# Optimization experiments

Hardware: AMD Instinct MI355X
Metric: run time of the kernel (lower is better)

The kernel has to match this reference:

```python
import jax, jax.numpy as jnp
import numpy as np

B, N, D, E = 16, 64, 512, 512
MSG = 512          # message_size must equal edge_feature_size (scatter into edge states)
LINK_H = 512       # GraphConv hidden channels
P = 2              # propagate_layers
HOI, ROLES = 26, 2


def setup_inputs() -> dict:
    key = jax.random.key(0)
    ks = jax.random.split(key, 12)
    s = 0.02
    return dict(
        edge_features=jax.random.normal(ks[0], (B, N, N, E), jnp.float32),
        node_features=jax.random.normal(ks[1], (B, N, D), jnp.float32),
        node_labels=jnp.zeros((B, N, HOI), jnp.float32),
        node_roles=jnp.zeros((B, N, ROLES), jnp.float32),
        # message_fun 'linear_concat_relu': Linear(D+E -> MSG) + ReLU
        Wm=(jax.random.normal(ks[2], (MSG, D + E), jnp.float32) * s),
        bm=jnp.zeros((MSG,), jnp.float32),
        # link_fun GraphConv: 1x1 Conv2d stack E->LINK_H->LINK_H->1
        Wl1=(jax.random.normal(ks[3], (LINK_H, E), jnp.float32) * s),
        bl1=jnp.zeros((LINK_H,), jnp.float32),
        Wl2=(jax.random.normal(ks[4], (LINK_H, LINK_H), jnp.float32) * s),
        bl2=jnp.zeros((LINK_H,), jnp.float32),
        Wlo=(jax.random.normal(ks[5], (1, LINK_H), jnp.float32) * s),
        blo=jnp.zeros((1,), jnp.float32),
        # update_fun GRU(input=MSG, hidden=D), torch gate order r,z,n
        W_ih=(jax.random.normal(ks[6], (3 * D, MSG), jnp.float32) * s),
        b_ih=jnp.zeros((3 * D,), jnp.float32),
        W_hh=(jax.random.normal(ks[7], (3 * D, D), jnp.float32) * s),
        b_hh=jnp.zeros((3 * D,), jnp.float32),
        # readout FCs
        Wr1=(jax.random.normal(ks[8], (HOI, D), jnp.float32) * s),
        br1=jnp.zeros((HOI,), jnp.float32),
        Wr2=(jax.random.normal(ks[9], (ROLES, D), jnp.float32) * s),
        br2=jnp.zeros((ROLES,), jnp.float32),
    )


def _link(x, Wl1, bl1, Wl2, bl2, Wlo, blo):
    # x: [B, C, N, N]; 1x1 conv stack -> [B, N, N]
    h = jax.nn.relu(jnp.einsum('bcvw,hc->bhvw', x, Wl1) + bl1[None, :, None, None])
    h = jax.nn.relu(jnp.einsum('bcvw,hc->bhvw', h, Wl2) + bl2[None, :, None, None])
    return (jnp.einsum('bcvw,hc->bhvw', h, Wlo) + blo[None, :, None, None])[:, 0]


def _forward(edge_features, node_features, Wm, bm, Wl1, bl1, Wl2, bl2, Wlo, blo,
             W_ih, b_ih, W_hh, b_hh, Wr1, br1, Wr2, br2):
    e = jnp.transpose(edge_features, (0, 3, 1, 2))   # [B,E,v,w]
    nf = jnp.transpose(node_features, (0, 2, 1))     # [B,D,N]
    # hidden node states are never written back in the source, so raw messages
    # m(h_w, e_vw) are constant across propagation rounds: compute once, vectorized over v.
    h_part = jnp.broadcast_to(nf[:, :, None, :], (B, D, N, N))   # h_w broadcast over v
    cat = jnp.concatenate([h_part, e], axis=1)                   # [B, D+E, v, w]
    M = jax.nn.relu(jnp.einsum('bcvw,mc->bmvw', cat, Wm) + bm[None, :, None, None])
    edge_state = e
    gated = M
    for _ in range(P):
        pred_adj = _link(edge_state, Wl1, bl1, Wl2, bl2, Wlo, blo)      # [B,v,w]
        gated = jax.nn.sigmoid(pred_adj)[:, None, :, :] * M            # [B,m,v,w]
        # source stores m_v into hidden_edge_states[..., :, :, i_node] (column v)
        edge_state = jnp.swapaxes(gated, 2, 3)
    m_sum = jnp.sum(gated, axis=3)                   # [B, m, v]
    x = jnp.swapaxes(m_sum, 1, 2)                    # [B, N, MSG] GRU input
    h = node_features                                # [B, N, D]  GRU hidden
    gi = x @ W_ih.T + b_ih
    gh = h @ W_hh.T + b_hh
    ir, iz, inn = jnp.split(gi, 3, axis=-1)
    hr, hz, hn = jnp.split(gh, 3, axis=-1)
    r = jax.nn.sigmoid(ir + hr)
    z = jax.nn.sigmoid(iz + hz)
    n = jnp.tanh(inn + r * hn)
    h_new = (1.0 - z) * n + z * h
    pred_node_labels = h_new @ Wr1.T + br1
    pred_node_roles = h_new @ Wr2.T + br2
    return pred_adj, pred_node_labels, pred_node_roles


def reference(edge_features, node_features, node_labels, node_roles, Wm, bm,
              Wl1, bl1, Wl2, bl2, Wlo, blo, W_ih, b_ih, W_hh, b_hh,
              Wr1, br1, Wr2, br2):
    return _forward(edge_features, node_features, Wm, bm, Wl1, bl1, Wl2, bl2,
                    Wlo, blo, W_ih, b_ih, W_hh, b_hh, Wr1, br1, Wr2, br2)
```

## Files before the change

kernel.cpp:

```cpp
#include <hip/hip_runtime.h>
#include <hip/hip_bf16.h>
#include <stdint.h>
#include <stddef.h>


using u16 = unsigned short;
using u32 = unsigned int;

__device__ __forceinline__ float u2f(u16 u) {
  union { unsigned i; float f; } c; c.i = ((unsigned)u) << 16; return c.f;
}
__device__ __forceinline__ u16 f2u(float f) {
  __hip_bfloat16 h = __float2bfloat16(f);
  union { __hip_bfloat16 h; u16 u; } c; c.h = h; return c.u;
}
__device__ __forceinline__ u32 pk2(float lo, float hi) {
  __hip_bfloat162 h = __float22bfloat162_rn(make_float2(lo, hi));
  union { __hip_bfloat162 h; u32 u; } c; c.h = h; return c.u;
}
__device__ __forceinline__ float sigm(float x) { return 1.f / (1.f + expf(-x)); }

typedef __attribute__((ext_vector_type(8))) short bfrag;
typedef __attribute__((ext_vector_type(4))) float f32x4;

__device__ __forceinline__ void gl_lds16(const u16* g, u16* l) {
  __builtin_amdgcn_global_load_lds((const __attribute__((address_space(1))) void*)g,
                                   (__attribute__((address_space(3))) void*)l,
                                   16, 0, 0);
}

#define NSEG 17
struct CvtArgs {
  const float* src[NSEG];
  u16* dst[NSEG];
  int cum[NSEG + 1];
};
__global__ __launch_bounds__(256) void cvt_multi(CvtArgs a, int total) {
  int i = blockIdx.x * 256 + threadIdx.x;
  if (i >= total) return;
  int s = 0;
  while (s + 1 < NSEG && i >= a.cum[s + 1]) ++s;
  const int off = i - a.cum[s];
  a.dst[s][off] = f2u(a.src[s][off]);
}

template <int MODE, bool A32>
__global__ __launch_bounds__(512, 2)
void gemm256(const void* __restrict__ Av, int lda, size_t abase,
             const u16* __restrict__ W, int ldw, int K,
             const u16* __restrict__ bias,
             const float* __restrict__ ubuf,
             const u16* __restrict__ wlo,
             float* __restrict__ pred,
             u16* __restrict__ outb, int ldc,
             const u16* __restrict__ W2, int ldw2, u16* __restrict__ outb2)
{
  __shared__ u16 smem[32768];
  u16* const As0 = smem;
  u16* const Bs0 = smem + 8192;
  u16* const As1 = smem + 16384;
  u16* const Bs1 = smem + 24576;

  const int tid  = threadIdx.x;
  const int wave = tid >> 6, lane = tid & 63;
  const int wr = wave >> 2, wc = wave & 3;
  const int quad = lane >> 4, l16 = lane & 15;
  const int swz = (quad ^ ((l16 >> 1) & 3)) << 3;

  const int gx = gridDim.x;
  const int nwg = gx * gridDim.y;
  int flat = blockIdx.y * gx + blockIdx.x;
  if ((nwg & 7) == 0) { const int q = nwg >> 3; flat = (flat & 7) * q + (flat >> 3); }
  const int bx = flat % gx;
  const int by = flat / gx;

  const int row0 = by * 256;
  const bool isM = (MODE != 5) || (bx < 2);
  const int col0 = (MODE == 5 ? (bx & 1) : bx) * 256;
  const u16* Wp  = (MODE == 5 && !isM) ? W2  : W;
  const int ldwp = (MODE == 5 && !isM) ? ldw2 : ldw;

  f32x4 acc[8][4];
#pragma unroll
  for (int i = 0; i < 8; i++)
#pragma unroll
    for (int j = 0; j < 4; j++)
#pragma unroll
      for (int r = 0; r < 4; r++) acc[i][j][r] = 0.f;

  auto stageB = [&](int k0, u16* Bb) {
#pragma unroll
    for (int p = 0; p < 2; p++) {
      const int idx = p * 512 + tid;
      const int row = idx >> 2;
      const int cb  = (idx & 3) ^ ((row >> 1) & 3);
      gl_lds16(Wp + (size_t)(col0 + row) * ldwp + k0 + cb * 8, Bb + idx * 8);
    }
  };
  auto stageA = [&](int k0, u16* Ab) {
#pragma unroll
    for (int p = 0; p < 2; p++) {
      const int idx = p * 512 + tid;
      const int row = idx >> 2;
      const int cb  = (idx & 3) ^ ((row >> 1) & 3);
      gl_lds16((const u16*)Av + (abase + (size_t)(row0 + row)) * lda + k0 + cb * 8,
               Ab + idx * 8);
    }
  };

  float4 rfa[2][4];

#define LOADRF(k0, S) {                                                          \
    const float* p_ = (const float*)Av +                                         \
        (abase + (size_t)(row0 + (tid >> 1))) * lda + (k0) + (tid & 1) * 16;     \
    rfa[S][0] = *(const float4*)p_;      rfa[S][1] = *(const float4*)(p_ + 4);   \
    rfa[S][2] = *(const float4*)(p_ + 8); rfa[S][3] = *(const float4*)(p_ + 12); }

#define WRITEA(S, Ab) {                                                          \
    const int r_ = tid >> 1, h_ = tid & 1;                                       \
    const int sw_ = (r_ >> 1) & 3;                                               \
    uint4 w0_, w1_;                                                              \
    w0_.x = pk2(rfa[S][0].x, rfa[S][0].y); w0_.y = pk2(rfa[S][0].z, rfa[S][0].w);\
    w0_.z = pk2(rfa[S][1].x, rfa[S][1].y); w0_.w = pk2(rfa[S][1].z, rfa[S][1].w);\
    w1_.x = pk2(rfa[S][2].x, rfa[S][2].y); w1_.y = pk2(rfa[S][2].z, rfa[S][2].w);\
    w1_.z = pk2(rfa[S][3].x, rfa[S][3].y); w1_.w = pk2(rfa[S][3].z, rfa[S][3].w);\
    *(uint4*)((Ab) + r_ * 32 + (((2 * h_) ^ sw_) << 3))     = w0_;               \
    *(uint4*)((Ab) + r_ * 32 + (((2 * h_ + 1) ^ sw_) << 3)) = w1_; }

  auto compute = [&](const u16* Ab, const u16* Bb) {
    bfrag af[8], bf[4];
#pragma unroll
    for (int mt = 0; mt < 8; mt++)
      af[mt] = *(const bfrag*)(Ab + wr * 4096 + mt * 512 + l16 * 32 + swz);
#pragma unroll
    for (int nt = 0; nt < 4; nt++)
      bf[nt] = *(const bfrag*)(Bb + wc * 2048 + nt * 512 + l16 * 32 + swz);
#pragma unroll
    for (int mt = 0; mt < 8; mt++)
#pragma unroll
      for (int nt = 0; nt < 4; nt++)
        acc[mt][nt] = __builtin_amdgcn_mfma_f32_16x16x32_bf16(af[mt], bf[nt], acc[mt][nt], 0, 0, 0);
  };

  const int ntile = K >> 5;

  if constexpr (A32) {
    LOADRF(0, 0);
    WRITEA(0, As0);
    stageB(0, Bs0);
    if (ntile > 1) LOADRF(32, 1);
  } else {
    stageA(0, As0);
    stageB(0, Bs0);
  }
  __syncthreads();

  for (int t = 0; t < ntile; t += 2) {
    {
      const bool more = (t + 1 < ntile);
      if (more) {
        stageB((t + 1) << 5, Bs1);
        if constexpr (!A32) stageA((t + 1) << 5, As1);
        if constexpr (A32) {
          WRITEA(1, As1);
          if (t + 2 < ntile) LOADRF((t + 2) << 5, 0);
        }
      }
      compute(As0, Bs0);
      __syncthreads();
    }
    if (t + 1 < ntile) {
      const bool more = (t + 2 < ntile);
      if (more) {
        stageB((t + 2) << 5, Bs0);
        if constexpr (!A32) stageA((t + 2) << 5, As0);
        if constexpr (A32) {
          WRITEA(0, As0);
          if (t + 3 < ntile) LOADRF((t + 3) << 5, 1);
        }
      }
      compute(As1, Bs1);
      __syncthreads();
    }
  }
#undef LOADRF
#undef WRITEA

  if constexpr (MODE == 2) {
#pragma unroll
    for (int mt = 0; mt < 8; mt++) {
#pragma unroll
      for (int r = 0; r < 4; r++) {
        const int rg = row0 + wr * 128 + mt * 16 + quad * 4 + r;
        float s = 0.f;
#pragma unroll
        for (int nt = 0; nt < 4; nt++) {
          const int cg = col0 + wc * 64 + nt * 16 + l16;
          float v = acc[mt][nt][r] + u2f(bias[cg]);
          v = fmaxf(v, 0.f);
          s += v * u2f(wlo[cg]);
        }
#pragma unroll
        for (int off = 1; off < 16; off <<= 1) s += __shfl_xor(s, off, 16);
        if (l16 == 0) atomicAdd(pred + rg, s);
      }
    }
  } else {
    u16* outp = (MODE == 5 && !isM) ? outb2 : outb;
    u16* tile = smem;
#pragma unroll
    for (int p = 0; p < 4; p++) {
      __syncthreads();
      if (wr == (p >> 1)) {
        const int mtb = (p & 1) * 4;
#pragma unroll
        for (int mi = 0; mi < 4; mi++) {
          const int mt = mtb + mi;
#pragma unroll
          for (int nt = 0; nt < 4; nt++)
#pragma unroll
            for (int r = 0; r < 4; r++) {
              const int rg = row0 + wr * 128 + mt * 16 + quad * 4 + r;
              const int cg = col0 + wc * 64 + nt * 16 + l16;
              float v = acc[mt][nt][r];
              if (MODE == 5 && isM) {
                const size_t grow = (size_t)rg;
                const int urow = (int)(((grow >> 12) << 6) | (grow & 63));
                v += ubuf[(size_t)urow * 512 + cg];
                v = fmaxf(v, 0.f);
              } else if (MODE == 5) {
                v += u2f(bias[cg]);
                v = fmaxf(v, 0.f);
              } else {
                v = sigm(pred[rg]) * v + u2f(bias[cg]);
                v = fmaxf(v, 0.f);
              }
              const int lrow = mt * 16 + quad * 4 + r - (p & 1) * 64;
              tile[lrow * 264 + wc * 64 + nt * 16 + l16] = f2u(v);
            }
        }
      }
      __syncthreads();
      const int row = tid >> 3, ch = tid & 7;
      const u16* src = tile + row * 264 + ch * 32;
      u16* dst = outp + (size_t)(row0 + p * 64 + row) * ldc + col0 + ch * 32;
#pragma unroll
      for (int j = 0; j < 4; j++)
        *(uint4*)(dst + j * 8) = *(const uint4*)(src + j * 8);
    }
  }
}

template <int MODE, bool A32>
__global__ __launch_bounds__(256)
void gemm_bt(const void* __restrict__ Av, int lda, size_t abase,
             const u16* __restrict__ W, int ldw, int K,
             const u16* __restrict__ bias,
             const float* __restrict__ ubuf,
             const u16* __restrict__ wlo,
             float* __restrict__ pred,
             u16* __restrict__ outb,
             float* __restrict__ outf,
             int ldc,
             const u16* __restrict__ W2, int ldw2, u16* __restrict__ outb2)
{
  __shared__ u16 smem[32768];
  u16* const Abase = smem;
  u16* const Bbase = smem + 16384;

  const int tid  = threadIdx.x;
  const int wave = tid >> 6, lane = tid & 63;
  const int wr = wave >> 1, wc = wave & 1;
  const int quad = lane >> 4, l16 = lane & 15;
  const int srow8 = lane >> 3;
  const int scolsw = ((lane & 7) ^ srow8) * 8;

  const int gx = gridDim.x;
  const int nwg = gx * gridDim.y;
  int flat = blockIdx.y * gx + blockIdx.x;
  if ((nwg & 7) == 0) { const int q = nwg >> 3; flat = (flat & 7) * q + (flat >> 3); }
  const int bx = flat % gx;
  const int by = flat / gx;

  const int row0 = by * 128;
  const bool isM = (MODE != 5) || (bx < 4);
  const int col0 = (MODE == 5 ? (bx & 3) : bx) * 128;
  const u16* Wp  = (MODE == 5 && !isM) ? W2  : W;
  const int ldwp = (MODE == 5 && !isM) ? ldw2 : ldw;

  f32x4 acc[4][4];
#pragma unroll
  for (int i = 0; i < 4; i++)
#pragma unroll
    for (int j = 0; j < 4; j++)
#pragma unroll
      for (int r = 0; r < 4; r++) acc[i][j][r] = 0.f;

  float4 rf[8];
  uint4  ra[4];

  auto stageA = [&](int kk0, u16* dst) {
#pragma unroll
    for (int i = 0; i < 4; i++) {
      const int chunk = wave * 4 + i;
      gl_lds16((const u16*)Av + (abase + (size_t)(row0 + chunk * 8 + srow8)) * lda + kk0 + scolsw,
               dst + chunk * 512 + lane * 8);
    }
  };
  auto stageB = [&](int kk0, u16* dst) {
#pragma unroll
    for (int i = 0; i < 4; i++) {
      const int chunk = wave * 4 + i;
      gl_lds16(Wp + (size_t)(col0 + chunk * 8 + srow8) * ldwp + kk0 + scolsw,
               dst + chunk * 512 + lane * 8);
    }
  };
  auto loadRF = [&](int kk0) {
#pragma unroll
    for (int i = 0; i < 4; i++) {
      const int idx = i * 256 + tid, sr = idx >> 3, sc = (idx & 7) * 8;
      const float* p = (const float*)Av + (abase + (size_t)(row0 + sr)) * lda + kk0 + sc;
      rf[2 * i]     = *(const float4*)p;
      rf[2 * i + 1] = *(const float4*)(p + 4);
    }
  };
  auto convRA = [&]() {
#pragma unroll
    for (int i = 0; i < 4; i++) {
      ra[i].x = pk2(rf[2 * i].x, rf[2 * i].y);
      ra[i].y = pk2(rf[2 * i].z, rf[2 * i].w);
      ra[i].z = pk2(rf[2 * i + 1].x, rf[2 * i + 1].y);
      ra[i].w = pk2(rf[2 * i + 1].z, rf[2 * i + 1].w);
    }
  };
  auto writeA = [&](u16* dst) {
#pragma unroll
    for (int i = 0; i < 4; i++) {
      const int idx = i * 256 + tid, sr = idx >> 3, cb = idx & 7;
      *(uint4*)(dst + sr * 64 + ((cb ^ (sr & 7)) << 3)) = ra[i];
    }
  };
  auto compute = [&](const u16* Ac, const u16* Bc) {
#pragma unroll
    for (int kk = 0; kk < 64; kk += 32) {
      const int cb0 = (kk >> 3) + quad;
      const int cbsw = ((cb0 ^ (l16 & 7)) << 3);
      bfrag af[4], bf[4];
#pragma unroll
      for (int mt = 0; mt < 4; mt++) {
        const int R = wr * 64 + mt * 16 + l16;
        af[mt] = *(const bfrag*)(Ac + R * 64 + cbsw);
      }
#pragma unroll
      for (int nt2 = 0; nt2 < 4; nt2++) {
        const int R = wc * 64 + nt2 * 16 + l16;
        bf[nt2] = *(const bfrag*)(Bc + R * 64 + cbsw);
      }
#pragma unroll
      for (int mt = 0; mt < 4; mt++)
#pragma unroll
        for (int nt2 = 0; nt2 < 4; nt2++)
          acc[mt][nt2] = __builtin_amdgcn_mfma_f32_16x16x32_bf16(af[mt], bf[nt2], acc[mt][nt2], 0, 0, 0);
    }
  };

  const int ntile = K >> 6;
  int cur = 0;

  if constexpr (A32) {
    loadRF(0); convRA(); writeA(Abase);
    stageB(0, Bbase);
    if (ntile > 1) loadRF(64);
  } else {
    stageA(0, Abase);
    stageB(0, Bbase);
  }
  __syncthreads();

  for (int t = 0; t < ntile; ++t) {
    const bool more = (t + 1 < ntile);
    u16* Ac = Abase + cur * 8192;
    u16* Bc = Bbase + cur * 8192;
    u16* An = Abase + (cur ^ 1) * 8192;
    u16* Bn = Bbase + (cur ^ 1) * 8192;
    if (more) {
      if constexpr (!A32) stageA((t + 1) << 6, An);
      stageB((t + 1) << 6, Bn);
      if constexpr (A32) {
        convRA(); writeA(An);
        if (t + 2 < ntile) loadRF((t + 2) << 6);
      }
    }
    compute(Ac, Bc);
    __syncthreads();
    cur ^= 1;
  }

  if constexpr (MODE == 2) {
#pragma unroll
    for (int mt = 0; mt < 4; mt++) {
#pragma unroll
      for (int r = 0; r < 4; r++) {
        const int rg = row0 + wr * 64 + mt * 16 + quad * 4 + r;
        float s = 0.f;
#pragma unroll
        for (int nt = 0; nt < 4; nt++) {
          const int cg = col0 + wc * 64 + nt * 16 + l16;
          float v = acc[mt][nt][r] + u2f(bias[cg]);
          v = fmaxf(v, 0.f);
          s += v * u2f(wlo[cg]);
        }
#pragma unroll
        for (int off = 1; off < 16; off <<= 1) s += __shfl_xor(s, off, 16);
        if (l16 == 0) atomicAdd(pred + rg, s);
      }
    }
  } else if constexpr (MODE == 3) {
#pragma unroll
    for (int mt = 0; mt < 4; mt++)
#pragma unroll
      for (int nt = 0; nt < 4; nt++)
#pragma unroll
        for (int r = 0; r < 4; r++) {
          const int rg = row0 + wr * 64 + mt * 16 + quad * 4 + r;
          const int cg = col0 + wc * 64 + nt * 16 + l16;
          outf[(size_t)rg * ldc + cg] = acc[mt][nt][r] + u2f(bias[cg]);
        }
  } else {
    u16* tile = smem;
    u16* outp = (MODE == 5 && !isM) ? outb2 : outb;
    __syncthreads();
#pragma unroll
    for (int mt = 0; mt < 4; mt++)
#pragma unroll
      for (int nt = 0; nt < 4; nt++)
#pragma unroll
        for (int r = 0; r < 4; r++) {
          const int lrow = wr * 64 + mt * 16 + quad * 4 + r;
          const int lcol = wc * 64 + nt * 16 + l16;
          const int rg = row0 + lrow;
          const int cg = col0 + lcol;
          float v = acc[mt][nt][r];
          if (MODE == 0 || (MODE == 5 && isM)) {
            const size_t grow = abase + rg;
            const int urow = (int)(((grow >> 12) << 6) | (grow & 63));
            v += ubuf[(size_t)urow * 512 + cg];
            v = fmaxf(v, 0.f);
          } else if (MODE == 1 || MODE == 5) {
            v += u2f(bias[cg]);
            v = fmaxf(v, 0.f);
          } else {
            v = sigm(pred[rg]) * v + u2f(bias[cg]);
            v = fmaxf(v, 0.f);
          }
          tile[lrow * 136 + lcol] = f2u(v);
        }
    __syncthreads();
    const int row = tid >> 1, half = tid & 1;
    const u16* src = tile + row * 136 + half * 64;
    u16* dst = outp + (size_t)(row0 + row) * ldc + col0 + half * 64;
#pragma unroll
    for (int j = 0; j < 8; j++)
      *(uint4*)(dst + j * 8) = *(const uint4*)(src + j * 8);
  }
}

__global__ void fill_kernel(float* __restrict__ p, const u16* __restrict__ val, int n) {
  int i = blockIdx.x * blockDim.x + threadIdx.x;
  if (i < n) p[i] = u2f(*val);
}

__global__ void adj_out_kernel(const float* __restrict__ r, float* __restrict__ out) {
  int i = blockIdx.x * 256 + threadIdx.x;
  int b = i >> 12, v = (i >> 6) & 63, w = i & 63;
  out[i] = r[(b << 12) + (w << 6) + v];
}

__global__ __launch_bounds__(512)
void msum_kernel(const float* __restrict__ r, const u16* __restrict__ M, u16* __restrict__ x) {
  const int bv = blockIdx.x;
  const int b = bv >> 6, v = bv & 63;
  __shared__ float s[64];
  if (threadIdx.x < 64) {
    const int w = threadIdx.x;
    s[w] = sigm(r[(b << 12) + (w << 6) + v]);
  }
  __syncthreads();
  const int m = threadIdx.x;
  const u16* Mp = M + (((size_t)(b << 12) + (v << 6)) << 9) + m;
  float acc = 0.f;
#pragma unroll 8
  for (int w = 0; w < 64; w++) acc += s[w] * u2f(Mp[(size_t)w << 9]);
  x[(size_t)bv * 512 + m] = f2u(acc);
}

__global__ __launch_bounds__(256)
void gru_kernel(const float* __restrict__ gi, const float* __restrict__ gh,
                const u16* __restrict__ h, float* __restrict__ hn) {
  int i = blockIdx.x * 256 + threadIdx.x;
  int row = i >> 9, d = i & 511;
  const float* gir = gi + (size_t)row * 1536;
  const float* ghr = gh + (size_t)row * 1536;
  float rr = sigm(gir[d] + ghr[d]);
  float z  = sigm(gir[512 + d] + ghr[512 + d]);
  float n  = tanhf(gir[1024 + d] + rr * ghr[1024 + d]);
  float hv = u2f(h[i]);
  hn[i] = (1.f - z) * n + z * hv;
}

__global__ __launch_bounds__(256)
void readout_kernel(const float* __restrict__ hn,
                    const u16* __restrict__ Wr1, const u16* __restrict__ br1,
                    const u16* __restrict__ Wr2, const u16* __restrict__ br2,
                    float* __restrict__ out) {
  const int row = blockIdx.x;
  __shared__ float hrow[512];
  for (int d = threadIdx.x; d < 512; d += 256) hrow[d] = hn[(size_t)row * 512 + d];
  __syncthreads();
  const int wave = threadIdx.x >> 6, lane = threadIdx.x & 63;
  for (int j = wave; j < 28; j += 4) {
    const u16* wrow;
    float bias;
    size_t off;
    if (j < 26) { wrow = Wr1 + (size_t)j * 512; bias = u2f(br1[j]); off = 65536 + (size_t)row * 26 + j; }
    else { int jj = j - 26; wrow = Wr2 + (size_t)jj * 512; bias = u2f(br2[jj]); off = 92160 + (size_t)row * 2 + jj; }
    float s = 0.f;
    for (int d = lane; d < 512; d += 64) s += hrow[d] * u2f(wrow[d]);
#pragma unroll
    for (int o = 32; o; o >>= 1) s += __shfl_down(s, o);
    if (lane == 0) out[off] = s + bias;
  }
}

extern "C" void kernel_launch(void* const* d_in, const int* in_sizes, int n_in,
                              void* d_out, int out_size, void* d_ws, size_t ws_size,
                              hipStream_t stream)
{
  (void)in_sizes; (void)n_in; (void)out_size;
  const void*  X  = d_in[0];
  char* ws = (char*)d_ws;

  const bool big = (ws_size >= 158905344ULL);

  u16 *Mb, *H1, *xb, *nfb, *Wmb, *bmb, *Wl1b, *bl1b, *Wl2b, *bl2b, *Wlob, *blob;
  u16 *Wihb, *bihb, *Whhb, *bhhb, *Wr1b, *br1b, *Wr2b, *br2b;
  float *pred1, *rbuf, *ubuf, *gi, *gh, *hn;
  if (big) {
    Mb    = (u16*)(ws);
    H1    = (u16*)(ws + 67108864);
    pred1 = (float*)(ws + 134217728);
    rbuf  = (float*)(ws + 134479872);
    ubuf  = (float*)(ws + 134742016);
    xb    = (u16*)(ws + 136839168);
    gi    = (float*)(ws + 137887744);
    gh    = (float*)(ws + 144179200);
    hn    = (float*)(ws + 150470656);
    nfb   = (u16*)(ws + 152567808);
    Wmb   = (u16*)(ws + 153616384);
    bmb   = (u16*)(ws + 154664960);
    Wl1b  = (u16*)(ws + 154665984);
    bl1b  = (u16*)(ws + 155190272);
    Wl2b  = (u16*)(ws + 155191296);
    bl2b  = (u16*)(ws + 155715584);
    Wlob  = (u16*)(ws + 155716608);
    blob  = (u16*)(ws + 155717632);
    Wihb  = (u16*)(ws + 155718656);
    bihb  = (u16*)(ws + 157291520);
    Whhb  = (u16*)(ws + 157295616);
    bhhb  = (u16*)(ws + 158868480);
    Wr1b  = (u16*)(ws + 158872576);
    br1b  = (u16*)(ws + 158901248);
    Wr2b  = (u16*)(ws + 158902272);
    br2b  = (u16*)(ws + 158904320);
  } else {
    Mb    = (u16*)(ws);
    H1    = (u16*)(ws + 67108864);
    pred1 = (float*)(ws + 83886080);
    rbuf  = (float*)(ws + 84148224);
    ubuf  = (float*)(ws + 84410368);
    xb    = (u16*)(ws + 86507520);
    gi    = (float*)(ws + 87556096);
    gh    = (float*)(ws + 93847552);
    hn    = (float*)(ws + 100139008);
    nfb   = (u16*)(ws + 102236416);
    Wmb   = (u16*)(ws + 103284992);
    bmb   = (u16*)(ws + 104333568);
    Wl1b  = (u16*)(ws + 104334592);
    bl1b  = (u16*)(ws + 104858880);
    Wl2b  = (u16*)(ws + 104859904);
    bl2b  = (u16*)(ws + 105384192);
    Wlob  = (u16*)(ws + 105385216);
    blob  = (u16*)(ws + 105386240);
    Wihb  = (u16*)(ws + 105387264);
    bihb  = (u16*)(ws + 106960128);
    Whhb  = (u16*)(ws + 106964224);
    bhhb  = (u16*)(ws + 108537088);
    Wr1b  = (u16*)(ws + 108541184);
    br1b  = (u16*)(ws + 108573952);
    Wr2b  = (u16*)(ws + 108574976);
    br2b  = (u16*)(ws + 108579072);
  }

  float* out = (float*)d_out;

  {
    CvtArgs ca;
    const int seg_in[NSEG]  = {1,4,5,6,7,8,9,10,11,12,13,14,15,16,17,18,19};
    u16* seg_dst[NSEG] = {nfb,Wmb,bmb,Wl1b,bl1b,Wl2b,bl2b,Wlob,blob,
                          Wihb,bihb,Whhb,bhhb,Wr1b,br1b,Wr2b,br2b};
    const int seg_n[NSEG] = {524288,524288,512,262144,512,262144,512,512,1,
                             786432,1536,786432,1536,13312,26,1024,2};
    int total = 0;
    for (int s = 0; s < NSEG; s++) {
      ca.src[s] = (const float*)d_in[seg_in[s]];
      ca.dst[s] = seg_dst[s];
      ca.cum[s] = total;
      total += seg_n[s];
    }
    ca.cum[NSEG] = total;
    cvt_multi<<<(total + 255) / 256, 256, 0, stream>>>(ca, total);
  }

  gemm_bt<3, false><<<dim3(4, 8), 256, 0, stream>>>(nfb, 512, 0, Wmb, 1024, 512, bmb,
      nullptr, nullptr, nullptr, nullptr, ubuf, 512, nullptr, 0, nullptr);
  fill_kernel<<<512, 256, 0, stream>>>(pred1, blob, 131072);

  if (big) {
    gemm256<5, true><<<dim3(4, 256), 512, 0, stream>>>(X, 512, 0, Wmb + 512, 1024, 512,
        bl1b, ubuf, nullptr, nullptr, Mb, 512, Wl1b, 512, H1);
    gemm256<2, false><<<dim3(2, 256), 512, 0, stream>>>(H1, 512, 0, Wl2b, 512, 512, bl2b,
        nullptr, Wlob, pred1, nullptr, 512, nullptr, 0, nullptr);
    gemm256<4, false><<<dim3(2, 256), 512, 0, stream>>>(Mb, 512, 0, Wl1b, 512, 512, bl1b,
        nullptr, nullptr, pred1, H1, 512, nullptr, 0, nullptr);
    gemm256<2, false><<<dim3(2, 256), 512, 0, stream>>>(H1, 512, 0, Wl2b, 512, 512, bl2b,
        nullptr, Wlob, rbuf, nullptr, 512, nullptr, 0, nullptr);
  } else {
    gemm_bt<0, true><<<dim3(4, 512), 256, 0, stream>>>(X, 512, 0, Wmb + 512, 1024, 512,
        nullptr, ubuf, nullptr, nullptr, Mb, nullptr, 512, nullptr, 0, nullptr);
    for (int q = 0; q < 4; q++) {
      const size_t ro = (size_t)q * 16384;
      gemm_bt<1, true><<<dim3(4, 128), 256, 0, stream>>>(X, 512, ro, Wl1b, 512, 512, bl1b,
          nullptr, nullptr, nullptr, H1, nullptr, 512, nullptr, 0, nullptr);
      gemm_bt<2, false><<<dim3(4, 128), 256, 0, stream>>>(H1, 512, 0, Wl2b, 512, 512, bl2b,
          nullptr, Wlob, pred1 + ro, nullptr, nullptr, 512, nullptr, 0, nullptr);
    }
    for (int q = 0; q < 4; q++) {
      const size_t ro = (size_t)q * 16384;
      gemm_bt<4, false><<<dim3(4, 128), 256, 0, stream>>>(Mb, 512, ro, Wl1b, 512, 512, bl1b,
          nullptr, nullptr, pred1 + ro, H1, nullptr, 512, nullptr, 0, nullptr);
      gemm_bt<2, false><<<dim3(4, 128), 256, 0, stream>>>(H1, 512, 0, Wl2b, 512, 512, bl2b,
          nullptr, Wlob, rbuf + ro, nullptr, nullptr, 512, nullptr, 0, nullptr);
    }
  }

  adj_out_kernel<<<256, 256, 0, stream>>>(rbuf, out);
  msum_kernel<<<1024, 512, 0, stream>>>(rbuf, Mb, xb);
  gemm_bt<3, false><<<dim3(12, 8), 256, 0, stream>>>(xb, 512, 0, Wihb, 512, 512, bihb,
      nullptr, nullptr, nullptr, nullptr, gi, 1536, nullptr, 0, nullptr);
  gemm_bt<3, false><<<dim3(12, 8), 256, 0, stream>>>(nfb, 512, 0, Whhb, 512, 512, bhhb,
      nullptr, nullptr, nullptr, nullptr, gh, 1536, nullptr, 0, nullptr);
  gru_kernel<<<2048, 256, 0, stream>>>(gi, gh, nfb, hn);
  readout_kernel<<<1024, 256, 0, stream>>>(hn, Wr1b, br1b, Wr2b, br2b, out);
}
```

Before: 696.9 us.

## Use 128x256 tiles with triple-buffered A and fine-grained vmcnt waits

The big-path GEMM kernel now uses 128-row by 256-column tiles instead of 256x256, which halves the accumulators per wave and doubles the grid. The bf16 path triple-buffers A and double-buffers B, and waits with explicit s_waitcnt vmcnt counts plus raw barriers in place of full __syncthreads. MFMA sections also get a raised wave priority. The aim is better latency hiding and occupancy, at the cost of reloading the weight tile twice as often.

```diff
diff --git a/kernel.cpp b/kernel.cpp
--- a/kernel.cpp
+++ b/kernel.cpp
@@ -46,7 +46,7 @@
 
 template <int MODE, bool A32>
 __global__ __launch_bounds__(512, 2)
-void gemm256(const void* __restrict__ Av, int lda, size_t abase,
+void gemm_p3(const void* __restrict__ Av, int lda, size_t abase,
              const u16* __restrict__ W, int ldw, int K,
              const u16* __restrict__ bias,
              const float* __restrict__ ubuf,
@@ -55,17 +55,14 @@
              u16* __restrict__ outb, int ldc,
              const u16* __restrict__ W2, int ldw2, u16* __restrict__ outb2)
 {
-  __shared__ u16 smem[32768];
-  u16* const As0 = smem;
-  u16* const Bs0 = smem + 8192;
-  u16* const As1 = smem + 16384;
-  u16* const Bs1 = smem + 24576;
+  __shared__ u16 smem[28672];
+  u16* const Ab0 = smem;
+  u16* const Bb0 = smem + 12288;
 
   const int tid  = threadIdx.x;
   const int wave = tid >> 6, lane = tid & 63;
   const int wr = wave >> 2, wc = wave & 3;
   const int quad = lane >> 4, l16 = lane & 15;
-  const int swz = (quad ^ ((l16 >> 1) & 3)) << 3;
 
   const int gx = gridDim.x;
   const int nwg = gx * gridDim.y;
@@ -74,124 +71,123 @@
   const int bx = flat % gx;
   const int by = flat / gx;
 
-  const int row0 = by * 256;
+  const int row0 = by * 128;
   const bool isM = (MODE != 5) || (bx < 2);
   const int col0 = (MODE == 5 ? (bx & 1) : bx) * 256;
   const u16* Wp  = (MODE == 5 && !isM) ? W2  : W;
   const int ldwp = (MODE == 5 && !isM) ? ldw2 : ldw;
 
-  f32x4 acc[8][4];
-#pragma unroll
-  for (int i = 0; i < 8; i++)
+  f32x4 acc[4][4];
+#pragma unroll
+  for (int i = 0; i < 4; i++)
 #pragma unroll
     for (int j = 0; j < 4; j++)
 #pragma unroll
       for (int r = 0; r < 4; r++) acc[i][j][r] = 0.f;
 
+  auto stageA = [&](int k0, u16* Ab) {
+    const int c = tid, r = c >> 2;
+    const int scb = (c & 3) ^ ((r >> 1) & 3);
+    gl_lds16((const u16*)Av + (abase + (size_t)(row0 + r)) * lda + k0 + scb * 8,
+             Ab + c * 8);
+  };
   auto stageB = [&](int k0, u16* Bb) {
 #pragma unroll
     for (int p = 0; p < 2; p++) {
-      const int idx = p * 512 + tid;
-      const int row = idx >> 2;
-      const int cb  = (idx & 3) ^ ((row >> 1) & 3);
-      gl_lds16(Wp + (size_t)(col0 + row) * ldwp + k0 + cb * 8, Bb + idx * 8);
-    }
-  };
-  auto stageA = [&](int k0, u16* Ab) {
-#pragma unroll
-    for (int p = 0; p < 2; p++) {
-      const int idx = p * 512 + tid;
-      const int row = idx >> 2;
-      const int cb  = (idx & 3) ^ ((row >> 1) & 3);
-      gl_lds16((const u16*)Av + (abase + (size_t)(row0 + row)) * lda + k0 + cb * 8,
-               Ab + idx * 8);
-    }
-  };
-
-  float4 rfa[2][4];
-
-#define LOADRF(k0, S) {                                                          \
-    const float* p_ = (const float*)Av +                                         \
-        (abase + (size_t)(row0 + (tid >> 1))) * lda + (k0) + (tid & 1) * 16;     \
-    rfa[S][0] = *(const float4*)p_;      rfa[S][1] = *(const float4*)(p_ + 4);   \
-    rfa[S][2] = *(const float4*)(p_ + 8); rfa[S][3] = *(const float4*)(p_ + 12); }
-
-#define WRITEA(S, Ab) {                                                          \
-    const int r_ = tid >> 1, h_ = tid & 1;                                       \
-    const int sw_ = (r_ >> 1) & 3;                                               \
-    uint4 w0_, w1_;                                                              \
-    w0_.x = pk2(rfa[S][0].x, rfa[S][0].y); w0_.y = pk2(rfa[S][0].z, rfa[S][0].w);\
-    w0_.z = pk2(rfa[S][1].x, rfa[S][1].y); w0_.w = pk2(rfa[S][1].z, rfa[S][1].w);\
-    w1_.x = pk2(rfa[S][2].x, rfa[S][2].y); w1_.y = pk2(rfa[S][2].z, rfa[S][2].w);\
-    w1_.z = pk2(rfa[S][3].x, rfa[S][3].y); w1_.w = pk2(rfa[S][3].z, rfa[S][3].w);\
-    *(uint4*)((Ab) + r_ * 32 + (((2 * h_) ^ sw_) << 3))     = w0_;               \
-    *(uint4*)((Ab) + r_ * 32 + (((2 * h_ + 1) ^ sw_) << 3)) = w1_; }
+      const int c = p * 512 + tid, r = c >> 2;
+      const int scb = (c & 3) ^ ((r >> 1) & 3);
+      gl_lds16(Wp + (size_t)(col0 + r) * ldwp + k0 + scb * 8, Bb + c * 8);
+    }
+  };
+
+  float4 rf0, rf1;
+  auto loadRF = [&](int k0) {
+    const float* p_ = (const float*)Av +
+        (abase + (size_t)(row0 + (tid >> 2))) * lda + k0 + (tid & 3) * 8;
+    rf0 = *(const float4*)p_;
+    rf1 = *(const float4*)(p_ + 4);
+  };
+  auto writeA = [&](u16* Ab) {
+    const int r = tid >> 2, cb = tid & 3;
+    uint4 w;
+    w.x = pk2(rf0.x, rf0.y); w.y = pk2(rf0.z, rf0.w);
+    w.z = pk2(rf1.x, rf1.y); w.w = pk2(rf1.z, rf1.w);
+    *(uint4*)(Ab + r * 32 + ((cb ^ ((r >> 1) & 3)) << 3)) = w;
+  };
 
   auto compute = [&](const u16* Ab, const u16* Bb) {
-    bfrag af[8], bf[4];
-#pragma unroll
-    for (int mt = 0; mt < 8; mt++)
-      af[mt] = *(const bfrag*)(Ab + wr * 4096 + mt * 512 + l16 * 32 + swz);
-#pragma unroll
-    for (int nt = 0; nt < 4; nt++)
-      bf[nt] = *(const bfrag*)(Bb + wc * 2048 + nt * 512 + l16 * 32 + swz);
-#pragma unroll
-    for (int mt = 0; mt < 8; mt++)
+    bfrag af[4], bf[4];
+#pragma unroll
+    for (int mt = 0; mt < 4; mt++) {
+      const int R = wr * 64 + mt * 16 + l16;
+      af[mt] = *(const bfrag*)(Ab + R * 32 + ((quad ^ ((R >> 1) & 3)) << 3));
+    }
+#pragma unroll
+    for (int nt = 0; nt < 4; nt++) {
+      const int R = wc * 64 + nt * 16 + l16;
+      bf[nt] = *(const bfrag*)(Bb + R * 32 + ((quad ^ ((R >> 1) & 3)) << 3));
+    }
+    __builtin_amdgcn_s_setprio(1);
+#pragma unroll
+    for (int mt = 0; mt < 4; mt++)
 #pragma unroll
       for (int nt = 0; nt < 4; nt++)
         acc[mt][nt] = __builtin_amdgcn_mfma_f32_16x16x32_bf16(af[mt], bf[nt], acc[mt][nt], 0, 0, 0);
-  };
-
-  const int ntile = K >> 5;
-
-  if constexpr (A32) {
-    LOADRF(0, 0);
-    WRITEA(0, As0);
-    stageB(0, Bs0);
-    if (ntile > 1) LOADRF(32, 1);
+    __builtin_amdgcn_s_setprio(0);
+  };
+
+  const int nt_ = K >> 5;
+
+  if constexpr (!A32) {
+    stageA(0, Ab0);
+    stageB(0, Bb0);
+    if (nt_ > 1) {
+      stageA(32, Ab0 + 4096);
+      asm volatile("s_waitcnt vmcnt(1)" ::: "memory");
+    } else {
+      asm volatile("s_waitcnt vmcnt(0)" ::: "memory");
+    }
+    __builtin_amdgcn_s_barrier();
+
+    for (int t = 0; t < nt_; ++t) {
+      if (t + 1 < nt_) stageB((t + 1) << 5, Bb0 + ((t + 1) & 1) * 8192);
+      if (t + 2 < nt_) stageA((t + 2) << 5, Ab0 + ((t + 2) % 3) * 4096);
+      compute(Ab0 + (t % 3) * 4096, Bb0 + (t & 1) * 8192);
+      if (t + 2 < nt_) { asm volatile("s_waitcnt vmcnt(1)" ::: "memory"); }
+      else             { asm volatile("s_waitcnt vmcnt(0)" ::: "memory"); }
+      __builtin_amdgcn_s_barrier();
+    }
   } else {
-    stageA(0, As0);
-    stageB(0, Bs0);
-  }
-  __syncthreads();
-
-  for (int t = 0; t < ntile; t += 2) {
-    {
-      const bool more = (t + 1 < ntile);
-      if (more) {
-        stageB((t + 1) << 5, Bs1);
-        if constexpr (!A32) stageA((t + 1) << 5, As1);
-        if constexpr (A32) {
-          WRITEA(1, As1);
-          if (t + 2 < ntile) LOADRF((t + 2) << 5, 0);
-        }
+    loadRF(0);
+    writeA(Ab0);
+    stageB(0, Bb0);
+    if (nt_ > 1) {
+      loadRF(32);
+      asm volatile("s_waitcnt vmcnt(2) lgkmcnt(0)" ::: "memory");
+    } else {
+      asm volatile("s_waitcnt vmcnt(0) lgkmcnt(0)" ::: "memory");
+    }
+    __builtin_amdgcn_s_barrier();
+
+    for (int t = 0; t < nt_; ++t) {
+      if (t + 1 < nt_) {
+        stageB((t + 1) << 5, Bb0 + ((t + 1) & 1) * 8192);
+        writeA(Ab0 + ((t + 1) & 1) * 4096);
       }
-      compute(As0, Bs0);
-      __syncthreads();
-    }
-    if (t + 1 < ntile) {
-      const bool more = (t + 2 < ntile);
-      if (more) {
-        stageB((t + 2) << 5, Bs0);
-        if constexpr (!A32) stageA((t + 2) << 5, As0);
-        if constexpr (A32) {
-          WRITEA(0, As0);
-          if (t + 3 < ntile) LOADRF((t + 3) << 5, 1);
-        }
-      }
-      compute(As1, Bs1);
-      __syncthreads();
-    }
-  }
-#undef LOADRF
-#undef WRITEA
+      if (t + 2 < nt_) loadRF((t + 2) << 5);
+      compute(Ab0 + (t & 1) * 4096, Bb0 + (t & 1) * 8192);
+      if (t + 2 < nt_) { asm volatile("s_waitcnt vmcnt(2) lgkmcnt(0)" ::: "memory"); }
+      else             { asm volatile("s_waitcnt vmcnt(0) lgkmcnt(0)" ::: "memory"); }
+      __builtin_amdgcn_s_barrier();
+    }
+  }
 
   if constexpr (MODE == 2) {
 #pragma unroll
-    for (int mt = 0; mt < 8; mt++) {
+    for (int mt = 0; mt < 4; mt++) {
 #pragma unroll
       for (int r = 0; r < 4; r++) {
-        const int rg = row0 + wr * 128 + mt * 16 + quad * 4 + r;
+        const int rg = row0 + wr * 64 + mt * 16 + quad * 4 + r;
         float s = 0.f;
 #pragma unroll
         for (int nt = 0; nt < 4; nt++) {
@@ -209,18 +205,16 @@
     u16* outp = (MODE == 5 && !isM) ? outb2 : outb;
     u16* tile = smem;
 #pragma unroll
-    for (int p = 0; p < 4; p++) {
+    for (int p = 0; p < 2; p++) {
       __syncthreads();
-      if (wr == (p >> 1)) {
-        const int mtb = (p & 1) * 4;
-#pragma unroll
-        for (int mi = 0; mi < 4; mi++) {
-          const int mt = mtb + mi;
+      if (wr == p) {
+#pragma unroll
+        for (int mt = 0; mt < 4; mt++)
 #pragma unroll
           for (int nt = 0; nt < 4; nt++)
 #pragma unroll
             for (int r = 0; r < 4; r++) {
-              const int rg = row0 + wr * 128 + mt * 16 + quad * 4 + r;
+              const int rg = row0 + p * 64 + mt * 16 + quad * 4 + r;
               const int cg = col0 + wc * 64 + nt * 16 + l16;
               float v = acc[mt][nt][r];
               if (MODE == 5 && isM) {
@@ -235,10 +229,9 @@
                 v = sigm(pred[rg]) * v + u2f(bias[cg]);
                 v = fmaxf(v, 0.f);
               }
-              const int lrow = mt * 16 + quad * 4 + r - (p & 1) * 64;
+              const int lrow = mt * 16 + quad * 4 + r;
               tile[lrow * 264 + wc * 64 + nt * 16 + l16] = f2u(v);
             }
-        }
       }
       __syncthreads();
       const int row = tid >> 3, ch = tid & 7;
@@ -626,13 +619,13 @@
   fill_kernel<<<512, 256, 0, stream>>>(pred1, blob, 131072);
 
   if (big) {
-    gemm256<5, true><<<dim3(4, 256), 512, 0, stream>>>(X, 512, 0, Wmb + 512, 1024, 512,
+    gemm_p3<5, true><<<dim3(4, 512), 512, 0, stream>>>(X, 512, 0, Wmb + 512, 1024, 512,
         bl1b, ubuf, nullptr, nullptr, Mb, 512, Wl1b, 512, H1);
-    gemm256<2, false><<<dim3(2, 256), 512, 0, stream>>>(H1, 512, 0, Wl2b, 512, 512, bl2b,
+    gemm_p3<2, false><<<dim3(2, 512), 512, 0, stream>>>(H1, 512, 0, Wl2b, 512, 512, bl2b,
         nullptr, Wlob, pred1, nullptr, 512, nullptr, 0, nullptr);
-    gemm256<4, false><<<dim3(2, 256), 512, 0, stream>>>(Mb, 512, 0, Wl1b, 512, 512, bl1b,
+    gemm_p3<4, false><<<dim3(2, 512), 512, 0, stream>>>(Mb, 512, 0, Wl1b, 512, 512, bl1b,
         nullptr, nullptr, pred1, H1, 512, nullptr, 0, nullptr);
-    gemm256<2, false><<<dim3(2, 256), 512, 0, stream>>>(H1, 512, 0, Wl2b, 512, 512, bl2b,
+    gemm_p3<2, false><<<dim3(2, 512), 512, 0, stream>>>(H1, 512, 0, Wl2b, 512, 512, bl2b,
         nullptr, Wlob, rbuf, nullptr, 512, nullptr, 0, nullptr);
   } else {
     gemm_bt<0, true><<<dim3(4, 512), 256, 0, stream>>>(X, 512, 0, Wmb + 512, 1024, 512,
```

After: 620.0 us. 11.0% less time.
